# Kernel tuning notes

Hardware: AMD Instinct MI355X
Metric: run time of the kernel (lower is better)

Reference implementation:

```python
import jax, jax.numpy as jnp
import numpy as np

TAU = 0.07
K = 50
EPS = 1e-8


def _flat_norm(x):
    # [B, C, H, W] -> [B*H*W, C], L2-normalized along C
    B, C = x.shape[0], x.shape[1]
    x = jnp.moveaxis(x, 1, -1).reshape(-1, C)
    n = jnp.linalg.norm(x, axis=-1, keepdims=True)
    return x / jnp.maximum(n, 1e-12)


def setup_inputs() -> dict:
    key = jax.random.key(0)
    ks = jax.random.split(key, 5)
    shp = (2, 128, 64, 64)
    lshp = (2, 4, 64, 64)
    return {
        "input": jax.random.normal(ks[0], shp, dtype=jnp.float32),
        "positive": jax.random.normal(ks[1], shp, dtype=jnp.float32),
        "negative": jax.random.normal(ks[2], shp, dtype=jnp.float32),
        "input_logits": jax.random.normal(ks[3], lshp, dtype=jnp.float32),
        "negative_logits": jax.random.normal(ks[4], lshp, dtype=jnp.float32),
    }


def reference(input, positive, negative, input_logits, negative_logits):
    norm_input = _flat_norm(input)        # [N, C]
    norm_positive = _flat_norm(positive)  # [N, C]
    norm_negative = _flat_norm(negative)  # [N, C]

    # check_input: multi-class logits branch (softmax over class dim, then max)
    in_probs = jax.nn.softmax(input_logits, axis=1)
    neg_probs = jax.nn.softmax(negative_logits, axis=1)
    seg_input = jnp.argmax(in_probs, axis=1).reshape(-1)       # [N] int
    seg_negative = jnp.argmax(neg_probs, axis=1).reshape(-1)   # [N] int
    negative_prob = jnp.max(neg_probs, axis=1).reshape(-1)     # [N] float

    # positive cosine similarity (unit vectors -> dot product)
    pos_sim = jnp.sum(norm_input * norm_positive, axis=-1)     # [N]

    # mask[i, j] = (seg_input[j] != seg_negative[i]) * negative_prob[i]
    diff = (seg_input[None, :] != seg_negative[:, None]).astype(jnp.float16)
    masked = diff.astype(jnp.float32) * negative_prob[:, None]  # [N, N]

    # top-k over dim=0 (negatives) for each input column j -> indices [N, K]
    _, idx = jax.lax.top_k(masked.T, K)                         # [N, K]
    sampled = norm_negative[idx]                                # [N, K, C]

    neg_sim = jnp.einsum('nkc,nc->nk', sampled, norm_input)     # [N, K]
    nominator = jnp.exp(pos_sim / TAU)                          # [N]
    denominator = jnp.sum(jnp.exp(neg_sim / TAU), axis=1) + nominator
    loss = -jnp.mean(jnp.log(nominator / (denominator + EPS)))

    alter_sim = jnp.einsum('nkc,nc->nk', sampled, norm_positive)
    alter_den = jnp.sum(jnp.exp(alter_sim / TAU), axis=1) + nominator
    alter_loss = -jnp.mean(jnp.log(nominator / (alter_den + EPS)))

    return loss + alter_loss
```

## Files before the change

### kernel.cpp

```cpp
#include <hip/hip_runtime.h>
#include <math.h>

#define TAU_INV (1.0f / 0.07f)
#define KSEL 50
#define KPAD 64
#define NPIX 8192
#define CCH 128
#define HWSZ 4096
#define NCLS 4
#define EPSL 1e-8f
#define NBINS 1026
#define PXT 32
#define SROW 132

__global__ void __launch_bounds__(256) mega_kernel(
        const float* __restrict__ input, const float* __restrict__ positive,
        const float* __restrict__ negative,
        const float* __restrict__ ilog, const float* __restrict__ nlog,
        float* __restrict__ ni, float* __restrict__ np_, float* __restrict__ nn,
        int* __restrict__ seg_in, int* __restrict__ seg_neg,
        float* __restrict__ neg_prob) {
    __shared__ float tile[CCH][65];
    __shared__ float partial[4][64];
    __shared__ float invn[64];

    int t = threadIdx.x;
    int blk = blockIdx.x;

    if (blk < 384) {
        int tensor = blk >> 7, chunk = blk & 127;
        const float* src = (tensor == 0) ? input : (tensor == 1) ? positive : negative;
        float*       dst = (tensor == 0) ? ni    : (tensor == 1) ? np_      : nn;

        int n0 = chunk * 64;
        int b = n0 >> 12, hw0 = n0 & (HWSZ - 1);
        const float* base = src + (size_t)b * CCH * HWSZ + hw0;

        #pragma unroll
        for (int i = 0; i < 8; ++i) {
            int lin = t + i * 256;
            int c = lin >> 4, hwq = (lin & 15) * 4;
            float4 v = *(const float4*)&base[(size_t)c * HWSZ + hwq];
            tile[c][hwq + 0] = v.x; tile[c][hwq + 1] = v.y;
            tile[c][hwq + 2] = v.z; tile[c][hwq + 3] = v.w;
        }
        __syncthreads();

        int nof = t & 63, part = t >> 6;
        float s = 0.f;
        #pragma unroll
        for (int j = 0; j < 32; ++j) {
            float v = tile[part * 32 + j][nof];
            s += v * v;
        }
        partial[part][nof] = s;
        __syncthreads();
        if (t < 64) {
            float tot = partial[0][t] + partial[1][t] + partial[2][t] + partial[3][t];
            invn[t] = 1.0f / fmaxf(sqrtf(tot), 1e-12f);
        }
        __syncthreads();

        #pragma unroll
        for (int i = 0; i < 8; ++i) {
            int lin = t + i * 256;
            int nf = lin >> 5, cq = (lin & 31) * 4;
            float inv = invn[nf];
            float4 o;
            o.x = tile[cq + 0][nf] * inv;
            o.y = tile[cq + 1][nf] * inv;
            o.z = tile[cq + 2][nf] * inv;
            o.w = tile[cq + 3][nf] * inv;
            *(float4*)&dst[(size_t)(n0 + nf) * CCH + cq] = o;
        }
    } else {
        int n0 = ((blk - 384) * 256 + t) * 4;
        int b = n0 >> 12, hw = n0 & (HWSZ - 1);

        const float* pi = ilog + (size_t)b * NCLS * HWSZ + hw;
        float4 a0 = *(const float4*)&pi[0];
        float4 a1 = *(const float4*)&pi[HWSZ];
        float4 a2 = *(const float4*)&pi[2 * HWSZ];
        float4 a3 = *(const float4*)&pi[3 * HWSZ];
        const float* pn = nlog + (size_t)b * NCLS * HWSZ + hw;
        float4 b0 = *(const float4*)&pn[0];
        float4 b1 = *(const float4*)&pn[HWSZ];
        float4 b2 = *(const float4*)&pn[2 * HWSZ];
        float4 b3 = *(const float4*)&pn[3 * HWSZ];

        int4 si4, sn4; float4 npb;
        const float* A0 = (const float*)&a0; const float* A1 = (const float*)&a1;
        const float* A2 = (const float*)&a2; const float* A3 = (const float*)&a3;
        const float* B0 = (const float*)&b0; const float* B1 = (const float*)&b1;
        const float* B2 = (const float*)&b2; const float* B3 = (const float*)&b3;
        int* SI = (int*)&si4; int* SN = (int*)&sn4; float* NP = (float*)&npb;
        #pragma unroll
        for (int j = 0; j < 4; ++j) {
            float l0 = A0[j], l1 = A1[j], l2 = A2[j], l3 = A3[j];
            int bi = 0; float bv = l0;
            if (l1 > bv) { bv = l1; bi = 1; }
            if (l2 > bv) { bv = l2; bi = 2; }
            if (l3 > bv) { bv = l3; bi = 3; }
            SI[j] = bi;
            float m0 = B0[j], m1 = B1[j], m2 = B2[j], m3 = B3[j];
            int ci = 0; float cv = m0;
            if (m1 > cv) { cv = m1; ci = 1; }
            if (m2 > cv) { cv = m2; ci = 2; }
            if (m3 > cv) { cv = m3; ci = 3; }
            SN[j] = ci;
            float s = expf(m0 - cv) + expf(m1 - cv) + expf(m2 - cv) + expf(m3 - cv);
            NP[j] = 1.0f / s;
        }
        *(int4*)&seg_in[n0] = si4;
        *(int4*)&seg_neg[n0] = sn4;
        *(float4*)&neg_prob[n0] = npb;
    }
}

__global__ void __launch_bounds__(1024) topk_kernel(
        const int* __restrict__ seg_in, const int* __restrict__ seg_neg,
        const float* __restrict__ neg_prob,
        int* __restrict__ topk, int* __restrict__ perm, int* __restrict__ cnt,
        float* __restrict__ out) {
    __shared__ unsigned hist[NBINS];
    __shared__ unsigned coarse[33];
    __shared__ unsigned long long cand[2048];
    __shared__ unsigned above_cnt, cand_cnt, bucket_cnt;
    __shared__ int sB, sc0;

    int c = blockIdx.x, t = threadIdx.x;
    if (c == 0 && t == 0) out[0] = 0.0f;

    for (int i = t; i < NBINS; i += 1024) hist[i] = 0;
    if (t < 33) coarse[t] = 0;
    if (t == 0) { above_cnt = 0; cand_cnt = 0; bucket_cnt = 0; }
    __syncthreads();

    unsigned keys[8]; int bins[8];
    #pragma unroll
    for (int s = 0; s < 2; ++s) {
        int i4 = (t + s * 1024) * 4;
        int4 sn = *(const int4*)&seg_neg[i4];
        int4 sg = *(const int4*)&seg_in[i4];
        float4 npv = *(const float4*)&neg_prob[i4];
        const int* SN = (const int*)&sn;
        const int* SG = (const int*)&sg;
        const float* NP = (const float*)&npv;
        #pragma unroll
        for (int j = 0; j < 4; ++j) {
            float v = (SN[j] != c) ? NP[j] : 0.0f;
            unsigned key = __float_as_uint(v);
            int bin = (key < 0x3E800000u) ? 0 : (int)(1u + ((key - 0x3E800000u) >> 14));
            keys[s * 4 + j] = key; bins[s * 4 + j] = bin;
            atomicAdd(&hist[bin], 1u);
            if (SG[j] == c) {
                unsigned p = atomicAdd(&bucket_cnt, 1u);
                perm[c * NPIX + p] = i4 + j;
            }
        }
    }
    __syncthreads();
    if (t == 0) cnt[c] = (int)bucket_cnt;

    for (int i = t; i < NBINS; i += 1024) atomicAdd(&coarse[i >> 5], hist[i]);
    __syncthreads();

    if (t == 0) {
        unsigned cum = 0; int j = 32;
        for (; j > 0; --j) {
            unsigned h = coarse[j];
            if (cum + h >= KSEL) break;
            cum += h;
        }
        int hi = j * 32 + 31; if (hi > NBINS - 1) hi = NBINS - 1;
        int B = 0;
        for (int b = hi; b >= j * 32; --b) {
            unsigned h = hist[b];
            if (cum + h >= KSEL) { B = b; break; }
            cum += h;
        }
        sB = B; sc0 = (int)cum;
    }
    __syncthreads();
    int B = sB, c0 = sc0;

    #pragma unroll
    for (int s = 0; s < 8; ++s) {
        int i = (t + (s >> 2) * 1024) * 4 + (s & 3);
        if (bins[s] > B) {
            unsigned pos = atomicAdd(&above_cnt, 1u);
            topk[c * KSEL + pos] = i;
        } else if (bins[s] == B) {
            unsigned j = atomicAdd(&cand_cnt, 1u);
            if (j < 2048)
                cand[j] = ((unsigned long long)keys[s] << 32) |
                          (unsigned long long)(0xFFFFFFFFu - (unsigned)i);
        }
    }
    __syncthreads();

    int m = KSEL - c0;
    int cb = (int)cand_cnt; if (cb > 2048) cb = 2048;
    if (t < 64) {
        for (int r = 0; r < m; ++r) {
            unsigned long long best = 0;
            for (int j = t; j < cb; j += 64) {
                unsigned long long v = cand[j];
                if (v > best) best = v;
            }
            #pragma unroll
            for (int off = 32; off; off >>= 1) {
                unsigned long long o = __shfl_xor(best, off);
                if (o > best) best = o;
            }
            if (t == 0) topk[c * KSEL + c0 + r] = (int)(0xFFFFFFFFu - (unsigned)(best & 0xFFFFFFFFull));
            for (int j = t; j < cb; j += 64)
                if (cand[j] == best) cand[j] = 0;
        }
    }
}

__global__ void __launch_bounds__(256) loss_kernel(
        const float* __restrict__ ni, const float* __restrict__ npos,
        const float* __restrict__ nn, const int* __restrict__ topk,
        const int* __restrict__ perm, const int* __restrict__ cnt,
        float* __restrict__ out) {
    __shared__ float Sl[KPAD * SROW];
    __shared__ float Xl[PXT * SROW];
    __shared__ float Pl[PXT * SROW];
    __shared__ float bsum[4];

    int c = blockIdx.y;
    int count = cnt[c];
    int start = blockIdx.x * PXT;
    if (start >= count) return;
    int t = threadIdx.x;

    {
        int row = t >> 2;
        int ch0 = (t & 3) * 32;
        float* dst = &Sl[row * SROW + ch0];
        if (row < KSEL) {
            const float* src = nn + (size_t)topk[c * KSEL + row] * CCH + ch0;
            #pragma unroll
            for (int i = 0; i < 8; ++i)
                ((float4*)dst)[i] = ((const float4*)src)[i];
        } else {
            float4 z = make_float4(0.f, 0.f, 0.f, 0.f);
            #pragma unroll
            for (int i = 0; i < 8; ++i)
                ((float4*)dst)[i] = z;
        }
    }
    {
        int row = t >> 3;
        int slot = start + row;
        int px = perm[c * NPIX + ((slot < count) ? slot : start)];
        int ch0 = (t & 7) * 16;
        const float* sx = ni + (size_t)px * CCH + ch0;
        const float* sp = npos + (size_t)px * CCH + ch0;
        float* dx = &Xl[row * SROW + ch0];
        float* dp = &Pl[row * SROW + ch0];
        #pragma unroll
        for (int i = 0; i < 4; ++i) {
            ((float4*)dx)[i] = ((const float4*)sx)[i];
            ((float4*)dp)[i] = ((const float4*)sp)[i];
        }
    }
    __syncthreads();

    int ktid = t & 7, pxid = t >> 3;
    float acc_i[8] = {0.f, 0.f, 0.f, 0.f, 0.f, 0.f, 0.f, 0.f};
    float acc_p[8] = {0.f, 0.f, 0.f, 0.f, 0.f, 0.f, 0.f, 0.f};
    float ps = 0.f;
    const float* Xr = &Xl[pxid * SROW];
    const float* Pr = &Pl[pxid * SROW];

    #pragma unroll 2
    for (int ch = 0; ch < CCH; ch += 4) {
        float4 xv = *(const float4*)&Xr[ch];
        float4 pv = *(const float4*)&Pr[ch];
        ps += xv.x * pv.x + xv.y * pv.y + xv.z * pv.z + xv.w * pv.w;
        #pragma unroll
        for (int r = 0; r < 8; ++r) {
            float4 sv = *(const float4*)&Sl[(ktid + r * 8) * SROW + ch];
            acc_i[r] += sv.x * xv.x + sv.y * xv.y + sv.z * xv.z + sv.w * xv.w;
            acc_p[r] += sv.x * pv.x + sv.y * pv.y + sv.z * pv.z + sv.w * pv.w;
        }
    }

    float si = 0.f, spp = 0.f;
    #pragma unroll
    for (int r = 0; r < 8; ++r) {
        si  += expf(acc_i[r] * TAU_INV);
        spp += expf(acc_p[r] * TAU_INV);
    }
    #pragma unroll
    for (int off = 1; off < 8; off <<= 1) {
        si  += __shfl_xor(si, off);
        spp += __shfl_xor(spp, off);
    }

    float v = 0.f;
    if (ktid == 0 && (start + pxid) < count) {
        si  -= (float)(KPAD - KSEL);
        spp -= (float)(KPAD - KSEL);
        float nom = expf(ps * TAU_INV);
        float li = -logf(nom / (si + nom + EPSL));
        float lp = -logf(nom / (spp + nom + EPSL));
        v = (li + lp) * (1.0f / (float)NPIX);
    }
    v += __shfl_xor(v, 8);
    v += __shfl_xor(v, 16);
    v += __shfl_xor(v, 32);
    int w = t >> 6;
    if ((t & 63) == 0) bsum[w] = v;
    __syncthreads();
    if (t == 0) atomicAdd(out, bsum[0] + bsum[1] + bsum[2] + bsum[3]);
}

extern "C" void kernel_launch(void* const* d_in, const int* in_sizes, int n_in,
                              void* d_out, int out_size, void* d_ws, size_t ws_size,
                              hipStream_t stream) {
    const float* input      = (const float*)d_in[0];
    const float* positive   = (const float*)d_in[1];
    const float* negative   = (const float*)d_in[2];
    const float* in_logits  = (const float*)d_in[3];
    const float* neg_logits = (const float*)d_in[4];
    float* out = (float*)d_out;

    float* ws  = (float*)d_ws;
    float* ni  = ws;
    float* np_ = ws + 1048576;
    float* nn  = ws + 2097152;
    int*   seg_in   = (int*)(ws + 3145728);
    int*   seg_neg  = seg_in + NPIX;
    float* neg_prob = (float*)(seg_neg + NPIX);
    int*   topk     = (int*)(neg_prob + NPIX);
    int*   cnt      = topk + 256;
    int*   perm     = cnt + 64;

    mega_kernel<<<392, 256, 0, stream>>>(input, positive, negative,
                                         in_logits, neg_logits,
                                         ni, np_, nn, seg_in, seg_neg, neg_prob);
    topk_kernel<<<NCLS, 1024, 0, stream>>>(seg_in, seg_neg, neg_prob,
                                           topk, perm, cnt, out);
    dim3 lgrid(NPIX / PXT, NCLS);
    loss_kernel<<<lgrid, 256, 0, stream>>>(ni, np_, nn, topk, perm, cnt, out);
}
```

Baseline: 99.72 us.

## Double pixel tile and use 4x4 register blocking in similarity loop

Raises the per-block pixel tile from 32 to 64 and restructures the compute loop so each thread holds a 4x4 block of (negative row, pixel) accumulators instead of 1 pixel by 8 negatives. This cuts shared-memory loads per FMA by reusing each loaded negative and pixel vector across several outputs, and halves the number of blocks that reload the 64-row negative tile. In exchange it uses more registers (32 accumulators plus 12 float4s), which may lower occupancy, and there are fewer blocks to spread across CUs.

```diff
diff --git a/kernel.cpp b/kernel.cpp
--- a/kernel.cpp
+++ b/kernel.cpp
@@ -10,7 +10,7 @@
 #define NCLS 4
 #define EPSL 1e-8f
 #define NBINS 1026
-#define PXT 32
+#define PXT 64
 #define SROW 132
 
 __global__ void __launch_bounds__(256) mega_kernel(
@@ -253,64 +253,92 @@
         }
     }
     {
-        int row = t >> 3;
+        int row = t >> 2;
         int slot = start + row;
         int px = perm[c * NPIX + ((slot < count) ? slot : start)];
-        int ch0 = (t & 7) * 16;
+        int ch0 = (t & 3) * 32;
         const float* sx = ni + (size_t)px * CCH + ch0;
         const float* sp = npos + (size_t)px * CCH + ch0;
         float* dx = &Xl[row * SROW + ch0];
         float* dp = &Pl[row * SROW + ch0];
         #pragma unroll
-        for (int i = 0; i < 4; ++i) {
+        for (int i = 0; i < 8; ++i) {
             ((float4*)dx)[i] = ((const float4*)sx)[i];
             ((float4*)dp)[i] = ((const float4*)sp)[i];
         }
     }
     __syncthreads();
 
-    int ktid = t & 7, pxid = t >> 3;
-    float acc_i[8] = {0.f, 0.f, 0.f, 0.f, 0.f, 0.f, 0.f, 0.f};
-    float acc_p[8] = {0.f, 0.f, 0.f, 0.f, 0.f, 0.f, 0.f, 0.f};
-    float ps = 0.f;
-    const float* Xr = &Xl[pxid * SROW];
-    const float* Pr = &Pl[pxid * SROW];
-
-    #pragma unroll 2
+    int ktid = t & 15, pxgrp = t >> 4;
+    float acc_i[4][4], acc_p[4][4], ps[4];
+    #pragma unroll
+    for (int r = 0; r < 4; ++r)
+        #pragma unroll
+        for (int p = 0; p < 4; ++p) { acc_i[r][p] = 0.f; acc_p[r][p] = 0.f; }
+    #pragma unroll
+    for (int p = 0; p < 4; ++p) ps[p] = 0.f;
+
     for (int ch = 0; ch < CCH; ch += 4) {
-        float4 xv = *(const float4*)&Xr[ch];
-        float4 pv = *(const float4*)&Pr[ch];
-        ps += xv.x * pv.x + xv.y * pv.y + xv.z * pv.z + xv.w * pv.w;
-        #pragma unroll
-        for (int r = 0; r < 8; ++r) {
-            float4 sv = *(const float4*)&Sl[(ktid + r * 8) * SROW + ch];
-            acc_i[r] += sv.x * xv.x + sv.y * xv.y + sv.z * xv.z + sv.w * xv.w;
-            acc_p[r] += sv.x * pv.x + sv.y * pv.y + sv.z * pv.z + sv.w * pv.w;
-        }
-    }
-
-    float si = 0.f, spp = 0.f;
-    #pragma unroll
-    for (int r = 0; r < 8; ++r) {
-        si  += expf(acc_i[r] * TAU_INV);
-        spp += expf(acc_p[r] * TAU_INV);
-    }
-    #pragma unroll
-    for (int off = 1; off < 8; off <<= 1) {
-        si  += __shfl_xor(si, off);
-        spp += __shfl_xor(spp, off);
+        float4 xv[4], pv[4], sv[4];
+        #pragma unroll
+        for (int p = 0; p < 4; ++p) {
+            xv[p] = *(const float4*)&Xl[(pxgrp + p * 16) * SROW + ch];
+            pv[p] = *(const float4*)&Pl[(pxgrp + p * 16) * SROW + ch];
+        }
+        #pragma unroll
+        for (int r = 0; r < 4; ++r)
+            sv[r] = *(const float4*)&Sl[(ktid + r * 16) * SROW + ch];
+
+        #pragma unroll
+        for (int p = 0; p < 4; ++p)
+            ps[p] += xv[p].x * pv[p].x + xv[p].y * pv[p].y +
+                     xv[p].z * pv[p].z + xv[p].w * pv[p].w;
+        #pragma unroll
+        for (int r = 0; r < 4; ++r) {
+            #pragma unroll
+            for (int p = 0; p < 4; ++p) {
+                acc_i[r][p] += sv[r].x * xv[p].x + sv[r].y * xv[p].y +
+                               sv[r].z * xv[p].z + sv[r].w * xv[p].w;
+                acc_p[r][p] += sv[r].x * pv[p].x + sv[r].y * pv[p].y +
+                               sv[r].z * pv[p].z + sv[r].w * pv[p].w;
+            }
+        }
+    }
+
+    float si[4], spp[4];
+    #pragma unroll
+    for (int p = 0; p < 4; ++p) { si[p] = 0.f; spp[p] = 0.f; }
+    #pragma unroll
+    for (int r = 0; r < 4; ++r) {
+        #pragma unroll
+        for (int p = 0; p < 4; ++p) {
+            si[p]  += expf(acc_i[r][p] * TAU_INV);
+            spp[p] += expf(acc_p[r][p] * TAU_INV);
+        }
+    }
+    #pragma unroll
+    for (int off = 1; off < 16; off <<= 1) {
+        #pragma unroll
+        for (int p = 0; p < 4; ++p) {
+            si[p]  += __shfl_xor(si[p], off);
+            spp[p] += __shfl_xor(spp[p], off);
+        }
     }
 
     float v = 0.f;
-    if (ktid == 0 && (start + pxid) < count) {
-        si  -= (float)(KPAD - KSEL);
-        spp -= (float)(KPAD - KSEL);
-        float nom = expf(ps * TAU_INV);
-        float li = -logf(nom / (si + nom + EPSL));
-        float lp = -logf(nom / (spp + nom + EPSL));
-        v = (li + lp) * (1.0f / (float)NPIX);
-    }
-    v += __shfl_xor(v, 8);
+    if (ktid == 0) {
+        #pragma unroll
+        for (int p = 0; p < 4; ++p) {
+            if ((start + pxgrp + p * 16) < count) {
+                float a = si[p]  - (float)(KPAD - KSEL);
+                float b = spp[p] - (float)(KPAD - KSEL);
+                float nom = expf(ps[p] * TAU_INV);
+                float li = -logf(nom / (a + nom + EPSL));
+                float lp = -logf(nom / (b + nom + EPSL));
+                v += (li + lp) * (1.0f / (float)NPIX);
+            }
+        }
+    }
     v += __shfl_xor(v, 16);
     v += __shfl_xor(v, 32);
     int w = t >> 6;
```

Result: no change. 100.7 us (+1.0%).

## Fuse normalize, top-k and loss into one cooperative kernel with grid syncs

Applied to the files above, without the earlier changes.

Merges the three launches (normalize/segment, per-class top-k, loss) into one cooperative kernel. It uses grid.sync between phases and a union of shared-memory layouts, so inter-kernel launch gaps are removed. The top-k phase now runs with 256 threads per block instead of 1024 and recomputes keys in its second pass rather than keeping them in registers. The loss phase uses 16-pixel tiles, each block looping over pixel slots with a persistent Sl tile. If the cooperative launch fails, it falls back to three separate launches; the risks are grid-sync overhead and a slower, less parallel top-k phase.

```diff
diff --git a/kernel.cpp b/kernel.cpp
--- a/kernel.cpp
+++ b/kernel.cpp
@@ -1,5 +1,8 @@
 #include <hip/hip_runtime.h>
+#include <hip/hip_cooperative_groups.h>
 #include <math.h>
+
+namespace cg = cooperative_groups;
 
 #define TAU_INV (1.0f / 0.07f)
 #define KSEL 50
@@ -10,22 +13,41 @@
 #define NCLS 4
 #define EPSL 1e-8f
 #define NBINS 1026
-#define PXT 32
+#define PXT 16
 #define SROW 132
 
-__global__ void __launch_bounds__(256) mega_kernel(
-        const float* __restrict__ input, const float* __restrict__ positive,
-        const float* __restrict__ negative,
-        const float* __restrict__ ilog, const float* __restrict__ nlog,
-        float* __restrict__ ni, float* __restrict__ np_, float* __restrict__ nn,
-        int* __restrict__ seg_in, int* __restrict__ seg_neg,
-        float* __restrict__ neg_prob) {
-    __shared__ float tile[CCH][65];
-    __shared__ float partial[4][64];
-    __shared__ float invn[64];
-
-    int t = threadIdx.x;
-    int blk = blockIdx.x;
+union SharedU {
+    struct {
+        float tile[CCH][65];
+        float partial[4][64];
+        float invn[64];
+    } a;
+    struct {
+        unsigned hist[NBINS];
+        unsigned coarse[33];
+        unsigned long long cand[2048];
+        unsigned above_cnt, cand_cnt, bucket_cnt;
+        int sB, sc0;
+    } b;
+    struct {
+        float Sl[KPAD * SROW];
+        float Xl[PXT * SROW];
+        float Pl[PXT * SROW];
+        float bsum[4];
+    } cst;
+};
+
+__device__ void phaseA(SharedU* sh, int blk, int t,
+                       const float* __restrict__ input,
+                       const float* __restrict__ positive,
+                       const float* __restrict__ negative,
+                       const float* __restrict__ ilog,
+                       const float* __restrict__ nlog,
+                       float* __restrict__ ni, float* __restrict__ np_,
+                       float* __restrict__ nn,
+                       int* __restrict__ seg_in, int* __restrict__ seg_neg,
+                       float* __restrict__ neg_prob, float* __restrict__ out) {
+    if (blk == 0 && t == 0) out[0] = 0.0f;
 
     if (blk < 384) {
         int tensor = blk >> 7, chunk = blk & 127;
@@ -41,8 +63,8 @@
             int lin = t + i * 256;
             int c = lin >> 4, hwq = (lin & 15) * 4;
             float4 v = *(const float4*)&base[(size_t)c * HWSZ + hwq];
-            tile[c][hwq + 0] = v.x; tile[c][hwq + 1] = v.y;
-            tile[c][hwq + 2] = v.z; tile[c][hwq + 3] = v.w;
+            sh->a.tile[c][hwq + 0] = v.x; sh->a.tile[c][hwq + 1] = v.y;
+            sh->a.tile[c][hwq + 2] = v.z; sh->a.tile[c][hwq + 3] = v.w;
         }
         __syncthreads();
 
@@ -50,14 +72,15 @@
         float s = 0.f;
         #pragma unroll
         for (int j = 0; j < 32; ++j) {
-            float v = tile[part * 32 + j][nof];
+            float v = sh->a.tile[part * 32 + j][nof];
             s += v * v;
         }
-        partial[part][nof] = s;
+        sh->a.partial[part][nof] = s;
         __syncthreads();
         if (t < 64) {
-            float tot = partial[0][t] + partial[1][t] + partial[2][t] + partial[3][t];
-            invn[t] = 1.0f / fmaxf(sqrtf(tot), 1e-12f);
+            float tot = sh->a.partial[0][t] + sh->a.partial[1][t] +
+                        sh->a.partial[2][t] + sh->a.partial[3][t];
+            sh->a.invn[t] = 1.0f / fmaxf(sqrtf(tot), 1e-12f);
         }
         __syncthreads();
 
@@ -65,15 +88,15 @@
         for (int i = 0; i < 8; ++i) {
             int lin = t + i * 256;
             int nf = lin >> 5, cq = (lin & 31) * 4;
-            float inv = invn[nf];
+            float inv = sh->a.invn[nf];
             float4 o;
-            o.x = tile[cq + 0][nf] * inv;
-            o.y = tile[cq + 1][nf] * inv;
-            o.z = tile[cq + 2][nf] * inv;
-            o.w = tile[cq + 3][nf] * inv;
+            o.x = sh->a.tile[cq + 0][nf] * inv;
+            o.y = sh->a.tile[cq + 1][nf] * inv;
+            o.z = sh->a.tile[cq + 2][nf] * inv;
+            o.w = sh->a.tile[cq + 3][nf] * inv;
             *(float4*)&dst[(size_t)(n0 + nf) * CCH + cq] = o;
         }
-    } else {
+    } else if (blk < 392) {
         int n0 = ((blk - 384) * 256 + t) * 4;
         int b = n0 >> 12, hw = n0 & (HWSZ - 1);
 
@@ -117,29 +140,20 @@
     }
 }
 
-__global__ void __launch_bounds__(1024) topk_kernel(
-        const int* __restrict__ seg_in, const int* __restrict__ seg_neg,
-        const float* __restrict__ neg_prob,
-        int* __restrict__ topk, int* __restrict__ perm, int* __restrict__ cnt,
-        float* __restrict__ out) {
-    __shared__ unsigned hist[NBINS];
-    __shared__ unsigned coarse[33];
-    __shared__ unsigned long long cand[2048];
-    __shared__ unsigned above_cnt, cand_cnt, bucket_cnt;
-    __shared__ int sB, sc0;
-
-    int c = blockIdx.x, t = threadIdx.x;
-    if (c == 0 && t == 0) out[0] = 0.0f;
-
-    for (int i = t; i < NBINS; i += 1024) hist[i] = 0;
-    if (t < 33) coarse[t] = 0;
-    if (t == 0) { above_cnt = 0; cand_cnt = 0; bucket_cnt = 0; }
-    __syncthreads();
-
-    unsigned keys[8]; int bins[8];
+__device__ void phaseB(SharedU* sh, int c, int t,
+                       const int* __restrict__ seg_in,
+                       const int* __restrict__ seg_neg,
+                       const float* __restrict__ neg_prob,
+                       int* __restrict__ topk, int* __restrict__ perm,
+                       int* __restrict__ cnt) {
+    for (int i = t; i < NBINS; i += 256) sh->b.hist[i] = 0;
+    if (t < 33) sh->b.coarse[t] = 0;
+    if (t == 0) { sh->b.above_cnt = 0; sh->b.cand_cnt = 0; sh->b.bucket_cnt = 0; }
+    __syncthreads();
+
     #pragma unroll
-    for (int s = 0; s < 2; ++s) {
-        int i4 = (t + s * 1024) * 4;
+    for (int s = 0; s < 8; ++s) {
+        int i4 = (t + s * 256) * 4;
         int4 sn = *(const int4*)&seg_neg[i4];
         int4 sg = *(const int4*)&seg_in[i4];
         float4 npv = *(const float4*)&neg_prob[i4];
@@ -151,61 +165,70 @@
             float v = (SN[j] != c) ? NP[j] : 0.0f;
             unsigned key = __float_as_uint(v);
             int bin = (key < 0x3E800000u) ? 0 : (int)(1u + ((key - 0x3E800000u) >> 14));
-            keys[s * 4 + j] = key; bins[s * 4 + j] = bin;
-            atomicAdd(&hist[bin], 1u);
+            atomicAdd(&sh->b.hist[bin], 1u);
             if (SG[j] == c) {
-                unsigned p = atomicAdd(&bucket_cnt, 1u);
+                unsigned p = atomicAdd(&sh->b.bucket_cnt, 1u);
                 perm[c * NPIX + p] = i4 + j;
             }
         }
     }
     __syncthreads();
-    if (t == 0) cnt[c] = (int)bucket_cnt;
-
-    for (int i = t; i < NBINS; i += 1024) atomicAdd(&coarse[i >> 5], hist[i]);
+    if (t == 0) cnt[c] = (int)sh->b.bucket_cnt;
+
+    for (int i = t; i < NBINS; i += 256) atomicAdd(&sh->b.coarse[i >> 5], sh->b.hist[i]);
     __syncthreads();
 
     if (t == 0) {
         unsigned cum = 0; int j = 32;
         for (; j > 0; --j) {
-            unsigned h = coarse[j];
+            unsigned h = sh->b.coarse[j];
             if (cum + h >= KSEL) break;
             cum += h;
         }
         int hi = j * 32 + 31; if (hi > NBINS - 1) hi = NBINS - 1;
         int B = 0;
         for (int b = hi; b >= j * 32; --b) {
-            unsigned h = hist[b];
+            unsigned h = sh->b.hist[b];
             if (cum + h >= KSEL) { B = b; break; }
             cum += h;
         }
-        sB = B; sc0 = (int)cum;
-    }
-    __syncthreads();
-    int B = sB, c0 = sc0;
+        sh->b.sB = B; sh->b.sc0 = (int)cum;
+    }
+    __syncthreads();
+    int B = sh->b.sB, c0 = sh->b.sc0;
 
     #pragma unroll
     for (int s = 0; s < 8; ++s) {
-        int i = (t + (s >> 2) * 1024) * 4 + (s & 3);
-        if (bins[s] > B) {
-            unsigned pos = atomicAdd(&above_cnt, 1u);
-            topk[c * KSEL + pos] = i;
-        } else if (bins[s] == B) {
-            unsigned j = atomicAdd(&cand_cnt, 1u);
-            if (j < 2048)
-                cand[j] = ((unsigned long long)keys[s] << 32) |
-                          (unsigned long long)(0xFFFFFFFFu - (unsigned)i);
+        int i4 = (t + s * 256) * 4;
+        int4 sn = *(const int4*)&seg_neg[i4];
+        float4 npv = *(const float4*)&neg_prob[i4];
+        const int* SN = (const int*)&sn;
+        const float* NP = (const float*)&npv;
+        #pragma unroll
+        for (int j = 0; j < 4; ++j) {
+            float v = (SN[j] != c) ? NP[j] : 0.0f;
+            unsigned key = __float_as_uint(v);
+            int bin = (key < 0x3E800000u) ? 0 : (int)(1u + ((key - 0x3E800000u) >> 14));
+            if (bin > B) {
+                unsigned pos = atomicAdd(&sh->b.above_cnt, 1u);
+                topk[c * KSEL + pos] = i4 + j;
+            } else if (bin == B) {
+                unsigned jj = atomicAdd(&sh->b.cand_cnt, 1u);
+                if (jj < 2048)
+                    sh->b.cand[jj] = ((unsigned long long)key << 32) |
+                                     (unsigned long long)(0xFFFFFFFFu - (unsigned)(i4 + j));
+            }
         }
     }
     __syncthreads();
 
     int m = KSEL - c0;
-    int cb = (int)cand_cnt; if (cb > 2048) cb = 2048;
+    int cb = (int)sh->b.cand_cnt; if (cb > 2048) cb = 2048;
     if (t < 64) {
         for (int r = 0; r < m; ++r) {
             unsigned long long best = 0;
             for (int j = t; j < cb; j += 64) {
-                unsigned long long v = cand[j];
+                unsigned long long v = sh->b.cand[j];
                 if (v > best) best = v;
             }
             #pragma unroll
@@ -215,31 +238,28 @@
             }
             if (t == 0) topk[c * KSEL + c0 + r] = (int)(0xFFFFFFFFu - (unsigned)(best & 0xFFFFFFFFull));
             for (int j = t; j < cb; j += 64)
-                if (cand[j] == best) cand[j] = 0;
-        }
-    }
-}
-
-__global__ void __launch_bounds__(256) loss_kernel(
-        const float* __restrict__ ni, const float* __restrict__ npos,
-        const float* __restrict__ nn, const int* __restrict__ topk,
-        const int* __restrict__ perm, const int* __restrict__ cnt,
-        float* __restrict__ out) {
-    __shared__ float Sl[KPAD * SROW];
-    __shared__ float Xl[PXT * SROW];
-    __shared__ float Pl[PXT * SROW];
-    __shared__ float bsum[4];
-
-    int c = blockIdx.y;
+                if (sh->b.cand[j] == best) sh->b.cand[j] = 0;
+        }
+    }
+}
+
+__device__ void phaseC(SharedU* sh, int blk, int t,
+                       const float* __restrict__ ni,
+                       const float* __restrict__ npos,
+                       const float* __restrict__ nn,
+                       const int* __restrict__ topk,
+                       const int* __restrict__ perm,
+                       const int* __restrict__ cnt,
+                       float* __restrict__ out) {
+    int c = blk & 3;
     int count = cnt[c];
-    int start = blockIdx.x * PXT;
-    if (start >= count) return;
-    int t = threadIdx.x;
+    int start0 = (blk >> 2) * PXT;
+    if (start0 >= count) return;
 
     {
         int row = t >> 2;
         int ch0 = (t & 3) * 32;
-        float* dst = &Sl[row * SROW + ch0];
+        float* dst = &sh->cst.Sl[row * SROW + ch0];
         if (row < KSEL) {
             const float* src = nn + (size_t)topk[c * KSEL + row] * CCH + ch0;
             #pragma unroll
@@ -252,71 +272,122 @@
                 ((float4*)dst)[i] = z;
         }
     }
-    {
-        int row = t >> 3;
-        int slot = start + row;
-        int px = perm[c * NPIX + ((slot < count) ? slot : start)];
-        int ch0 = (t & 7) * 16;
-        const float* sx = ni + (size_t)px * CCH + ch0;
-        const float* sp = npos + (size_t)px * CCH + ch0;
-        float* dx = &Xl[row * SROW + ch0];
-        float* dp = &Pl[row * SROW + ch0];
-        #pragma unroll
-        for (int i = 0; i < 4; ++i) {
-            ((float4*)dx)[i] = ((const float4*)sx)[i];
-            ((float4*)dp)[i] = ((const float4*)sp)[i];
-        }
-    }
-    __syncthreads();
-
-    int ktid = t & 7, pxid = t >> 3;
-    float acc_i[8] = {0.f, 0.f, 0.f, 0.f, 0.f, 0.f, 0.f, 0.f};
-    float acc_p[8] = {0.f, 0.f, 0.f, 0.f, 0.f, 0.f, 0.f, 0.f};
-    float ps = 0.f;
-    const float* Xr = &Xl[pxid * SROW];
-    const float* Pr = &Pl[pxid * SROW];
-
-    #pragma unroll 2
-    for (int ch = 0; ch < CCH; ch += 4) {
-        float4 xv = *(const float4*)&Xr[ch];
-        float4 pv = *(const float4*)&Pr[ch];
-        ps += xv.x * pv.x + xv.y * pv.y + xv.z * pv.z + xv.w * pv.w;
-        #pragma unroll
-        for (int r = 0; r < 8; ++r) {
-            float4 sv = *(const float4*)&Sl[(ktid + r * 8) * SROW + ch];
-            acc_i[r] += sv.x * xv.x + sv.y * xv.y + sv.z * xv.z + sv.w * xv.w;
-            acc_p[r] += sv.x * pv.x + sv.y * pv.y + sv.z * pv.z + sv.w * pv.w;
-        }
-    }
-
-    float si = 0.f, spp = 0.f;
-    #pragma unroll
-    for (int r = 0; r < 8; ++r) {
-        si  += expf(acc_i[r] * TAU_INV);
-        spp += expf(acc_p[r] * TAU_INV);
-    }
-    #pragma unroll
-    for (int off = 1; off < 8; off <<= 1) {
-        si  += __shfl_xor(si, off);
-        spp += __shfl_xor(spp, off);
-    }
-
-    float v = 0.f;
-    if (ktid == 0 && (start + pxid) < count) {
-        si  -= (float)(KPAD - KSEL);
-        spp -= (float)(KPAD - KSEL);
-        float nom = expf(ps * TAU_INV);
-        float li = -logf(nom / (si + nom + EPSL));
-        float lp = -logf(nom / (spp + nom + EPSL));
-        v = (li + lp) * (1.0f / (float)NPIX);
-    }
-    v += __shfl_xor(v, 8);
+
+    int ktid = t & 15, pxid = t >> 4;
+    float vtot = 0.f;
+
+    for (int start = start0; start < count; start += 128 * PXT) {
+        {
+            int row = t >> 4;
+            int slot = start + row;
+            int px = perm[c * NPIX + ((slot < count) ? slot : start)];
+            int ch0 = (t & 15) * 8;
+            const float* sx = ni + (size_t)px * CCH + ch0;
+            const float* sp = npos + (size_t)px * CCH + ch0;
+            float* dx = &sh->cst.Xl[row * SROW + ch0];
+            float* dp = &sh->cst.Pl[row * SROW + ch0];
+            ((float4*)dx)[0] = ((const float4*)sx)[0];
+            ((float4*)dx)[1] = ((const float4*)sx)[1];
+            ((float4*)dp)[0] = ((const float4*)sp)[0];
+            ((float4*)dp)[1] = ((const float4*)sp)[1];
+        }
+        __syncthreads();
+
+        float acc_i[4] = {0.f, 0.f, 0.f, 0.f};
+        float acc_p[4] = {0.f, 0.f, 0.f, 0.f};
+        float ps = 0.f;
+        const float* Xr = &sh->cst.Xl[pxid * SROW];
+        const float* Pr = &sh->cst.Pl[pxid * SROW];
+
+        #pragma unroll 4
+        for (int ch = 0; ch < CCH; ch += 4) {
+            float4 xv = *(const float4*)&Xr[ch];
+            float4 pv = *(const float4*)&Pr[ch];
+            ps += xv.x * pv.x + xv.y * pv.y + xv.z * pv.z + xv.w * pv.w;
+            #pragma unroll
+            for (int r = 0; r < 4; ++r) {
+                float4 sv = *(const float4*)&sh->cst.Sl[(ktid + r * 16) * SROW + ch];
+                acc_i[r] += sv.x * xv.x + sv.y * xv.y + sv.z * xv.z + sv.w * xv.w;
+                acc_p[r] += sv.x * pv.x + sv.y * pv.y + sv.z * pv.z + sv.w * pv.w;
+            }
+        }
+
+        float si = 0.f, spp = 0.f;
+        #pragma unroll
+        for (int r = 0; r < 4; ++r) {
+            si  += expf(acc_i[r] * TAU_INV);
+            spp += expf(acc_p[r] * TAU_INV);
+        }
+        #pragma unroll
+        for (int off = 1; off < 16; off <<= 1) {
+            si  += __shfl_xor(si, off);
+            spp += __shfl_xor(spp, off);
+        }
+
+        if (ktid == 0 && (start + pxid) < count) {
+            si  -= (float)(KPAD - KSEL);
+            spp -= (float)(KPAD - KSEL);
+            float nom = expf(ps * TAU_INV);
+            float li = -logf(nom / (si + nom + EPSL));
+            float lp = -logf(nom / (spp + nom + EPSL));
+            vtot += (li + lp) * (1.0f / (float)NPIX);
+        }
+        __syncthreads();
+    }
+
+    float v = vtot;
+    v += __shfl_xor(v, 1);
+    v = vtot;
     v += __shfl_xor(v, 16);
     v += __shfl_xor(v, 32);
     int w = t >> 6;
-    if ((t & 63) == 0) bsum[w] = v;
-    __syncthreads();
-    if (t == 0) atomicAdd(out, bsum[0] + bsum[1] + bsum[2] + bsum[3]);
+    if ((t & 63) == 0) sh->cst.bsum[w] = v;
+    __syncthreads();
+    if (t == 0) {
+        float s = sh->cst.bsum[0] + sh->cst.bsum[1] + sh->cst.bsum[2] + sh->cst.bsum[3];
+        atomicAdd(out, s);
+    }
+}
+
+__global__ void __launch_bounds__(256) fused_kernel(
+        const float* input, const float* positive, const float* negative,
+        const float* ilog, const float* nlog,
+        float* ni, float* np_, float* nn,
+        int* seg_in, int* seg_neg, float* neg_prob,
+        int* topk, int* perm, int* cnt, float* out) {
+    __shared__ SharedU sh;
+    int blk = blockIdx.x, t = threadIdx.x;
+    cg::grid_group grid = cg::this_grid();
+
+    phaseA(&sh, blk, t, input, positive, negative, ilog, nlog,
+           ni, np_, nn, seg_in, seg_neg, neg_prob, out);
+    grid.sync();
+    if (blk < NCLS)
+        phaseB(&sh, blk, t, seg_in, seg_neg, neg_prob, topk, perm, cnt);
+    grid.sync();
+    phaseC(&sh, blk, t, ni, np_, nn, topk, perm, cnt, out);
+}
+
+__global__ void __launch_bounds__(256) megaA_kernel(
+        const float* input, const float* positive, const float* negative,
+        const float* ilog, const float* nlog,
+        float* ni, float* np_, float* nn,
+        int* seg_in, int* seg_neg, float* neg_prob, float* out) {
+    __shared__ SharedU sh;
+    phaseA(&sh, blockIdx.x, threadIdx.x, input, positive, negative, ilog, nlog,
+           ni, np_, nn, seg_in, seg_neg, neg_prob, out);
+}
+__global__ void __launch_bounds__(256) topkB_kernel(
+        const int* seg_in, const int* seg_neg, const float* neg_prob,
+        int* topk, int* perm, int* cnt) {
+    __shared__ SharedU sh;
+    phaseB(&sh, blockIdx.x, threadIdx.x, seg_in, seg_neg, neg_prob, topk, perm, cnt);
+}
+__global__ void __launch_bounds__(256) lossC_kernel(
+        const float* ni, const float* npos, const float* nn,
+        const int* topk, const int* perm, const int* cnt, float* out) {
+    __shared__ SharedU sh;
+    phaseC(&sh, blockIdx.x, threadIdx.x, ni, npos, nn, topk, perm, cnt, out);
 }
 
 extern "C" void kernel_launch(void* const* d_in, const int* in_sizes, int n_in,
@@ -340,11 +411,23 @@
     int*   cnt      = topk + 256;
     int*   perm     = cnt + 64;
 
-    mega_kernel<<<392, 256, 0, stream>>>(input, positive, negative,
-                                         in_logits, neg_logits,
-                                         ni, np_, nn, seg_in, seg_neg, neg_prob);
-    topk_kernel<<<NCLS, 1024, 0, stream>>>(seg_in, seg_neg, neg_prob,
-                                           topk, perm, cnt, out);
-    dim3 lgrid(NPIX / PXT, NCLS);
-    loss_kernel<<<lgrid, 256, 0, stream>>>(ni, np_, nn, topk, perm, cnt, out);
-}
+    void* args[] = {
+        (void*)&input, (void*)&positive, (void*)&negative,
+        (void*)&in_logits, (void*)&neg_logits,
+        (void*)&ni, (void*)&np_, (void*)&nn,
+        (void*)&seg_in, (void*)&seg_neg, (void*)&neg_prob,
+        (void*)&topk, (void*)&perm, (void*)&cnt, (void*)&out
+    };
+    hipError_t e = hipLaunchCooperativeKernel((const void*)fused_kernel,
+                                              dim3(512), dim3(256),
+                                              args, 0, stream);
+    if (e != hipSuccess) {
+        megaA_kernel<<<392, 256, 0, stream>>>(input, positive, negative,
+                                              in_logits, neg_logits,
+                                              ni, np_, nn, seg_in, seg_neg,
+                                              neg_prob, out);
+        topkB_kernel<<<NCLS, 256, 0, stream>>>(seg_in, seg_neg, neg_prob,
+                                               topk, perm, cnt);
+        lossC_kernel<<<512, 256, 0, stream>>>(ni, np_, nn, topk, perm, cnt, out);
+    }
+}
```

Result: slower. 228.1 us (+128.8%).
